# Optimization experiments

Measured on AMD Instinct MI355X. Metric: run time of the kernel, lower is better.

The kernel has to match this reference:

```python
import jax, jax.numpy as jnp
import numpy as np

T_IN, T_OUT = 336, 96      # encoder window, output_length
B, D, H = 2048, 64, 512    # batch, input_size==output_size, hidden_size


def setup_inputs() -> dict:
    key = jax.random.key(0)
    ks = jax.random.split(key, 11)
    s = 0.04  # ~1/sqrt(H) init scale
    f32 = jnp.float32
    return {
        "inputs": jax.random.normal(ks[0], (T_IN, B, D), f32),
        "enc_Wih": jax.random.normal(ks[1], (4 * H, D), f32) * s,
        "enc_Whh": jax.random.normal(ks[2], (4 * H, H), f32) * s,
        "enc_bih": jax.random.normal(ks[3], (4 * H,), f32) * s,
        "enc_bhh": jax.random.normal(ks[4], (4 * H,), f32) * s,
        "dec_Wih": jax.random.normal(ks[5], (4 * H, D), f32) * s,
        "dec_Whh": jax.random.normal(ks[6], (4 * H, H), f32) * s,
        "dec_bih": jax.random.normal(ks[7], (4 * H,), f32) * s,
        "dec_bhh": jax.random.normal(ks[8], (4 * H,), f32) * s,
        "lin_W": jax.random.normal(ks[9], (D, H), f32) * s,
        "lin_b": jax.random.normal(ks[10], (D,), f32) * s,
    }


def _lstm_cell(h, c, x, Wih, Whh, b):
    # PyTorch gate order: i, f, g, o
    g = x @ Wih.T + h @ Whh.T + b          # [B, 4H]
    i, f, gg, o = jnp.split(g, 4, axis=-1)
    c = jax.nn.sigmoid(f) * c + jax.nn.sigmoid(i) * jnp.tanh(gg)
    h = jax.nn.sigmoid(o) * jnp.tanh(c)
    return h, c


def reference(inputs, enc_Wih, enc_Whh, enc_bih, enc_bhh,
              dec_Wih, dec_Whh, dec_bih, dec_bhh, lin_W, lin_b):
    Bsz = inputs.shape[1]
    dt = inputs.dtype
    h0 = jnp.zeros((Bsz, H), dt)
    c0 = jnp.zeros((Bsz, H), dt)

    enc_b = enc_bih + enc_bhh
    def enc_step(carry, x):
        h, c = carry
        h, c = _lstm_cell(h, c, x, enc_Wih, enc_Whh, enc_b)
        return (h, c), None
    (h, c), _ = jax.lax.scan(enc_step, (h0, c0), inputs)

    dec_b = dec_bih + dec_bhh
    x0 = jnp.zeros((Bsz, D), dt)  # decoder starts from zeros(1, B, output_size)
    def dec_step(carry, _):
        h, c, x = carry
        h, c = _lstm_cell(h, c, x, dec_Wih, dec_Whh, dec_b)
        y = h @ lin_W.T + lin_b
        x_next = jax.lax.stop_gradient(y)  # decoder_output.detach()
        return (h, c, x_next), y
    _, ys = jax.lax.scan(dec_step, (h, c, x0), None, length=T_OUT)
    return ys  # [T_OUT, B, D] == torch.cat(outputs, dim=0)
```

## Files before the change

### kernel.cpp

```cpp
#include <hip/hip_runtime.h>
#include <cstdint>
#include <cstddef>

typedef __bf16 bf16_t;
typedef __bf16 bf16x8 __attribute__((ext_vector_type(8)));
typedef __bf16 bf16x4 __attribute__((ext_vector_type(4)));
typedef float f32x4 __attribute__((ext_vector_type(4)));

#define N_TIN 336
#define N_TOUT 96
#define N_B   2048
#define N_D   64
#define N_H   512

__device__ __forceinline__ void llds16(const void* g, void* l) {
  __builtin_amdgcn_global_load_lds(
      (const __attribute__((address_space(1))) unsigned*)g,
      (__attribute__((address_space(3))) unsigned*)l, 16, 0, 0);
}
__device__ __forceinline__ float sigmf(float x) { return 1.0f / (1.0f + __expf(-x)); }
__device__ __forceinline__ float tanhft(float x) {
  x = fminf(15.0f, fmaxf(-15.0f, x));
  float e = __expf(2.0f * x);
  return (e - 1.0f) / (e + 1.0f);
}
__device__ __forceinline__ int perm_row(int m) {
  int j_hi = m >> 8;
  int fi   = (m >> 4) & 15;
  int c    = m & 15;
  int gate = fi & 3;
  int j    = j_hi * 64 + (fi >> 2) * 16 + c;
  return gate * N_H + j;
}

__global__ void prep_enc_w(const float* __restrict__ Wih, const float* __restrict__ Whh,
                           const float* __restrict__ bih, const float* __restrict__ bhh,
                           bf16_t* __restrict__ Wp, float* __restrict__ bp) {
  int m = blockIdx.x;
  int n = perm_row(m);
  for (int k = threadIdx.x; k < 576; k += 256) {
    float v = (k < 64) ? Wih[n * 64 + k] : Whh[n * 512 + (k - 64)];
    Wp[(size_t)m * 576 + k] = (bf16_t)v;
  }
  if (threadIdx.x == 0) bp[m] = bih[n] + bhh[n];
}

__global__ void prep_dec_w(const float* __restrict__ Wih, const float* __restrict__ Whh,
                           const float* __restrict__ bih, const float* __restrict__ bhh,
                           const float* __restrict__ linW, const float* __restrict__ linb,
                           bf16_t* __restrict__ W0p, bf16_t* __restrict__ Wep,
                           float* __restrict__ b0p, float* __restrict__ bep) {
  int m = blockIdx.x;
  int n = perm_row(m);
  for (int k = threadIdx.x; k < 512; k += 256) {
    float whh = Whh[n * 512 + k];
    W0p[(size_t)m * 512 + k] = (bf16_t)whh;
    float acc = whh;
    #pragma unroll 8
    for (int d = 0; d < 64; ++d) acc += Wih[n * 64 + d] * linW[d * 512 + k];
    Wep[(size_t)m * 512 + k] = (bf16_t)acc;
  }
  if (threadIdx.x == 0) {
    float b = bih[n] + bhh[n];
    b0p[m] = b;
    float acc = b;
    for (int d = 0; d < 64; ++d) acc += Wih[n * 64 + d] * linb[d];
    bep[m] = acc;
  }
}

__global__ void cvt_bf16_v4(const float* __restrict__ src, bf16_t* __restrict__ dst, int n4) {
  int i = blockIdx.x * 256 + threadIdx.x;
  int stride = gridDim.x * 256;
  for (; i < n4; i += stride) {
    float4 v = ((const float4*)src)[i];
    bf16x4 o;
    o[0] = (bf16_t)v.x; o[1] = (bf16_t)v.y; o[2] = (bf16_t)v.z; o[3] = (bf16_t)v.w;
    *(bf16x4*)(dst + (size_t)i * 4) = o;
  }
}

template<int KTOT, int XK>
__global__ __launch_bounds__(256, 1)
void lstm_step(const bf16_t* __restrict__ x,
               const bf16_t* __restrict__ h_in,
               const bf16_t* __restrict__ Wp,
               const float* __restrict__ bp,
               float* __restrict__ c,
               bf16_t* __restrict__ h_out) {
  __shared__ __align__(16) char smem[2 * 8192 + 2 * 32768];
  constexpr int NK = KTOT / 64;
  const int tid  = threadIdx.x;
  const int lane = tid & 63;
  const int w    = tid >> 6;
  const int row0 = blockIdx.x * 64;
  const int wg_n = blockIdx.y;
  const int l3 = lane >> 3;
  const int q8 = ((lane & 7) ^ l3) * 8;

  auto stage = [&](int kc, int buf) {
    char* Ab = smem + buf * 8192;
    char* Bb = smem + 16384 + buf * 32768;
    #pragma unroll
    for (int ii = 0; ii < 2; ++ii) {
      int i  = 2 * w + ii;
      int rl = i * 8 + l3;
      const bf16_t* src;
      if (XK != 0 && kc == 0)
        src = x + (size_t)(row0 + rl) * XK + q8;
      else
        src = h_in + (size_t)(row0 + rl) * N_H + (kc * 64 - XK) + q8;
      llds16(src, Ab + i * 1024);
    }
    #pragma unroll
    for (int jj = 0; jj < 8; ++jj) {
      int j  = 8 * w + jj;
      int nl = j * 8 + l3;
      const bf16_t* src = Wp + (size_t)(wg_n * 256 + nl) * KTOT + kc * 64 + q8;
      llds16(src, Bb + j * 1024);
    }
  };

  f32x4 acc[4][4];
  #pragma unroll
  for (int a = 0; a < 4; ++a)
    #pragma unroll
    for (int b = 0; b < 4; ++b) acc[a][b] = (f32x4){0.f, 0.f, 0.f, 0.f};

  const int fr = lane & 15;
  const int g4 = lane >> 4;
  const int px = lane & 7;

  stage(0, 0);
  for (int kc = 0; kc < NK; ++kc) {
    asm volatile("s_waitcnt vmcnt(0)" ::: "memory");
    __syncthreads();
    if (kc + 1 < NK) stage(kc + 1, (kc + 1) & 1);
    const char* Ab = smem + (kc & 1) * 8192;
    const char* Bb = smem + 16384 + (kc & 1) * 32768;
    #pragma unroll
    for (int kk = 0; kk < 2; ++kk) {
      bf16x8 av[4], bv[4];
      int p = (kk * 4 + g4) ^ px;
      #pragma unroll
      for (int ri = 0; ri < 4; ++ri)
        av[ri] = *(const bf16x8*)(Ab + (16 * ri + fr) * 128 + p * 16);
      #pragma unroll
      for (int ci = 0; ci < 4; ++ci)
        bv[ci] = *(const bf16x8*)(Bb + ((4 * w + ci) * 16 + fr) * 128 + p * 16);
      #pragma unroll
      for (int ri = 0; ri < 4; ++ri)
        #pragma unroll
        for (int ci = 0; ci < 4; ++ci)
          acc[ri][ci] = __builtin_amdgcn_mfma_f32_16x16x32_bf16(av[ri], bv[ci], acc[ri][ci], 0, 0, 0);
    }
  }

  const int jg = wg_n * 64 + w * 16 + fr;
  const int mb = wg_n * 256 + (4 * w) * 16 + fr;
  const float bI = bp[mb], bF = bp[mb + 16], bG = bp[mb + 32], bO = bp[mb + 48];
  #pragma unroll
  for (int ri = 0; ri < 4; ++ri) {
    #pragma unroll
    for (int r = 0; r < 4; ++r) {
      int rowl = 16 * ri + g4 * 4 + r;
      size_t idx = (size_t)(row0 + rowl) * N_H + jg;
      float iv = sigmf(acc[ri][0][r] + bI);
      float fv = sigmf(acc[ri][1][r] + bF);
      float gv = tanhft(acc[ri][2][r] + bG);
      float ov = sigmf(acc[ri][3][r] + bO);
      float cn = fv * c[idx] + iv * gv;
      c[idx] = cn;
      h_out[idx] = (bf16_t)(ov * tanhft(cn));
    }
  }
}

__global__ __launch_bounds__(256, 1)
void proj_y(const bf16_t* __restrict__ h,
            const bf16_t* __restrict__ Wl,
            const float* __restrict__ bl,
            float* __restrict__ y) {
  __shared__ __align__(16) char smem[4 * 8192];
  const int tid = threadIdx.x;
  const int lane = tid & 63;
  const int w = tid >> 6;
  const int row0 = blockIdx.x * 64;
  const int l3 = lane >> 3;
  const int q8 = ((lane & 7) ^ l3) * 8;

  auto stage = [&](int kc, int buf) {
    char* Ab = smem + buf * 8192;
    char* Bb = smem + 16384 + buf * 8192;
    #pragma unroll
    for (int ii = 0; ii < 2; ++ii) {
      int i = 2 * w + ii;
      int rl = i * 8 + l3;
      llds16(h  + (size_t)(row0 + rl) * N_H + kc * 64 + q8, Ab + i * 1024);
      llds16(Wl + (size_t)rl * N_H + kc * 64 + q8,          Bb + i * 1024);
    }
  };

  f32x4 acc[4];
  #pragma unroll
  for (int ci = 0; ci < 4; ++ci) acc[ci] = (f32x4){0.f, 0.f, 0.f, 0.f};
  const int fr = lane & 15, g4 = lane >> 4, px = lane & 7;

  stage(0, 0);
  for (int kc = 0; kc < 8; ++kc) {
    asm volatile("s_waitcnt vmcnt(0)" ::: "memory");
    __syncthreads();
    if (kc + 1 < 8) stage(kc + 1, (kc + 1) & 1);
    const char* Ab = smem + (kc & 1) * 8192;
    const char* Bb = smem + 16384 + (kc & 1) * 8192;
    #pragma unroll
    for (int kk = 0; kk < 2; ++kk) {
      int p = (kk * 4 + g4) ^ px;
      bf16x8 av = *(const bf16x8*)(Ab + (16 * w + fr) * 128 + p * 16);
      #pragma unroll
      for (int ci = 0; ci < 4; ++ci) {
        bf16x8 bv = *(const bf16x8*)(Bb + (ci * 16 + fr) * 128 + p * 16);
        acc[ci] = __builtin_amdgcn_mfma_f32_16x16x32_bf16(av, bv, acc[ci], 0, 0, 0);
      }
    }
  }
  #pragma unroll
  for (int ci = 0; ci < 4; ++ci) {
    float bb = bl[ci * 16 + fr];
    #pragma unroll
    for (int r = 0; r < 4; ++r) {
      int row = row0 + 16 * w + g4 * 4 + r;
      y[(size_t)row * N_D + ci * 16 + fr] = acc[ci][r] + bb;
    }
  }
}

extern "C" void kernel_launch(void* const* d_in, const int* in_sizes, int n_in,
                              void* d_out, int out_size, void* d_ws, size_t ws_size,
                              hipStream_t stream) {
  (void)in_sizes; (void)n_in; (void)out_size; (void)ws_size;
  const float* x_f  = (const float*)d_in[0];
  const float* eWih = (const float*)d_in[1];
  const float* eWhh = (const float*)d_in[2];
  const float* ebih = (const float*)d_in[3];
  const float* ebhh = (const float*)d_in[4];
  const float* dWih = (const float*)d_in[5];
  const float* dWhh = (const float*)d_in[6];
  const float* dbih = (const float*)d_in[7];
  const float* dbhh = (const float*)d_in[8];
  const float* linW = (const float*)d_in[9];
  const float* linb = (const float*)d_in[10];
  float* out = (float*)d_out;

  char* ws = (char*)d_ws;
  size_t off = 0;
  auto alloc = [&](size_t bytes) {
    char* p = ws + off;
    off += (bytes + 255) & ~(size_t)255;
    return p;
  };
  bf16_t* Wenc  = (bf16_t*)alloc(2048ull * 576 * 2);
  bf16_t* Wdec0 = (bf16_t*)alloc(2048ull * 512 * 2);
  bf16_t* Weff  = (bf16_t*)alloc(2048ull * 512 * 2);
  bf16_t* linWb = (bf16_t*)alloc(64ull * 512 * 2);
  float*  benc  = (float*)alloc(2048 * 4);
  float*  bdec0 = (float*)alloc(2048 * 4);
  float*  beff  = (float*)alloc(2048 * 4);
  bf16_t* xb    = (bf16_t*)alloc((size_t)N_TIN * N_B * N_D * 2);
  bf16_t* h_a   = (bf16_t*)alloc((size_t)N_B * N_H * 2);
  bf16_t* h_b   = (bf16_t*)alloc((size_t)N_B * N_H * 2);
  float*  cbuf  = (float*)alloc((size_t)N_B * N_H * 4);

  prep_enc_w<<<2048, 256, 0, stream>>>(eWih, eWhh, ebih, ebhh, Wenc, benc);
  prep_dec_w<<<2048, 256, 0, stream>>>(dWih, dWhh, dbih, dbhh, linW, linb,
                                       Wdec0, Weff, bdec0, beff);
  cvt_bf16_v4<<<32, 256, 0, stream>>>(linW, linWb, 64 * 512 / 4);
  cvt_bf16_v4<<<2048, 256, 0, stream>>>(x_f, xb, N_TIN * N_B * N_D / 4);
  hipMemsetAsync(h_a, 0, (size_t)N_B * N_H * 2, stream);
  hipMemsetAsync(cbuf, 0, (size_t)N_B * N_H * 4, stream);

  dim3 grid(32, 8);
  for (int t = 0; t < N_TIN; ++t) {
    const bf16_t* hi = (t & 1) ? h_b : h_a;
    bf16_t* ho = (t & 1) ? h_a : h_b;
    lstm_step<576, 64><<<grid, 256, 0, stream>>>(xb + (size_t)t * N_B * N_D,
                                                 hi, Wenc, benc, cbuf, ho);
  }
  for (int t = 0; t < N_TOUT; ++t) {
    const bf16_t* hi = (t & 1) ? h_b : h_a;
    bf16_t* ho = (t & 1) ? h_a : h_b;
    const bf16_t* W  = (t == 0) ? Wdec0 : Weff;
    const float*  bb = (t == 0) ? bdec0 : beff;
    lstm_step<512, 0><<<grid, 256, 0, stream>>>(nullptr, hi, W, bb, cbuf, ho);
    proj_y<<<32, 256, 0, stream>>>(ho, linWb, linb, out + (size_t)t * N_B * N_D);
  }
}
```

Baseline: 5.627 ms.

## Replace per-step launches with a persistent LSTM kernel using grid barriers

Replaces 432 separate lstm_step launches and 96 proj_y launches with one persistent kernel of 256 blocks. Each block keeps its slice of the recurrent weights in LDS for the whole sequence, keeps the cell state in registers, and synchronises steps with an atomic grid barrier. The y projection is overlapped into the next decoder step by designated waves. This removes launch overhead, repeated weight reloads and the c-state memory traffic. It relies on all 256 blocks being co-resident, and the barrier has a timeout that silently gives up rather than deadlocking.

New measurement: 11.61 ms. +106.3%, slower.

```diff
diff --git a/kernel.cpp b/kernel.cpp
--- a/kernel.cpp
+++ b/kernel.cpp
@@ -12,60 +12,23 @@
 #define N_B   2048
 #define N_D   64
 #define N_H   512
-
-__device__ __forceinline__ void llds16(const void* g, void* l) {
-  __builtin_amdgcn_global_load_lds(
-      (const __attribute__((address_space(1))) unsigned*)g,
-      (__attribute__((address_space(3))) unsigned*)l, 16, 0, 0);
-}
+#define NBLK  256
+
 __device__ __forceinline__ float sigmf(float x) { return 1.0f / (1.0f + __expf(-x)); }
 __device__ __forceinline__ float tanhft(float x) {
   x = fminf(15.0f, fmaxf(-15.0f, x));
   float e = __expf(2.0f * x);
   return (e - 1.0f) / (e + 1.0f);
 }
-__device__ __forceinline__ int perm_row(int m) {
-  int j_hi = m >> 8;
-  int fi   = (m >> 4) & 15;
-  int c    = m & 15;
-  int gate = fi & 3;
-  int j    = j_hi * 64 + (fi >> 2) * 16 + c;
-  return gate * N_H + j;
-}
-
-__global__ void prep_enc_w(const float* __restrict__ Wih, const float* __restrict__ Whh,
-                           const float* __restrict__ bih, const float* __restrict__ bhh,
-                           bf16_t* __restrict__ Wp, float* __restrict__ bp) {
-  int m = blockIdx.x;
-  int n = perm_row(m);
-  for (int k = threadIdx.x; k < 576; k += 256) {
-    float v = (k < 64) ? Wih[n * 64 + k] : Whh[n * 512 + (k - 64)];
-    Wp[(size_t)m * 576 + k] = (bf16_t)v;
-  }
-  if (threadIdx.x == 0) bp[m] = bih[n] + bhh[n];
-}
-
-__global__ void prep_dec_w(const float* __restrict__ Wih, const float* __restrict__ Whh,
-                           const float* __restrict__ bih, const float* __restrict__ bhh,
-                           const float* __restrict__ linW, const float* __restrict__ linb,
-                           bf16_t* __restrict__ W0p, bf16_t* __restrict__ Wep,
-                           float* __restrict__ b0p, float* __restrict__ bep) {
-  int m = blockIdx.x;
-  int n = perm_row(m);
-  for (int k = threadIdx.x; k < 512; k += 256) {
-    float whh = Whh[n * 512 + k];
-    W0p[(size_t)m * 512 + k] = (bf16_t)whh;
-    float acc = whh;
+
+__global__ void prep_weff(const float* __restrict__ dWih, const float* __restrict__ dWhh,
+                          const float* __restrict__ linW, bf16_t* __restrict__ Weff) {
+  int n = blockIdx.x;
+  for (int k = threadIdx.x; k < N_H; k += 256) {
+    float acc = dWhh[(size_t)n * N_H + k];
     #pragma unroll 8
-    for (int d = 0; d < 64; ++d) acc += Wih[n * 64 + d] * linW[d * 512 + k];
-    Wep[(size_t)m * 512 + k] = (bf16_t)acc;
-  }
-  if (threadIdx.x == 0) {
-    float b = bih[n] + bhh[n];
-    b0p[m] = b;
-    float acc = b;
-    for (int d = 0; d < 64; ++d) acc += Wih[n * 64 + d] * linb[d];
-    bep[m] = acc;
+    for (int d = 0; d < 64; ++d) acc += dWih[(size_t)n * 64 + d] * linW[(size_t)d * N_H + k];
+    Weff[(size_t)n * N_H + k] = (bf16_t)acc;
   }
 }
 
@@ -80,159 +43,207 @@
   }
 }
 
-template<int KTOT, int XK>
-__global__ __launch_bounds__(256, 1)
-void lstm_step(const bf16_t* __restrict__ x,
-               const bf16_t* __restrict__ h_in,
-               const bf16_t* __restrict__ Wp,
-               const float* __restrict__ bp,
-               float* __restrict__ c,
-               bf16_t* __restrict__ h_out) {
-  __shared__ __align__(16) char smem[2 * 8192 + 2 * 32768];
-  constexpr int NK = KTOT / 64;
+__global__ __launch_bounds__(512, 1)
+void lstm_persist(const bf16_t* __restrict__ xb,
+                  const float* __restrict__ eWih, const float* __restrict__ eWhh,
+                  const float* __restrict__ ebih, const float* __restrict__ ebhh,
+                  const float* __restrict__ dWih, const float* __restrict__ dWhh,
+                  const float* __restrict__ dbih, const float* __restrict__ dbhh,
+                  const float* __restrict__ linb, const bf16_t* __restrict__ Weff,
+                  const bf16_t* __restrict__ linWb,
+                  bf16_t* __restrict__ hb0, bf16_t* __restrict__ hb1,
+                  float* __restrict__ out, unsigned* bar)
+{
+  __shared__ __align__(16) char smem[16 * 8192];
   const int tid  = threadIdx.x;
   const int lane = tid & 63;
   const int w    = tid >> 6;
-  const int row0 = blockIdx.x * 64;
-  const int wg_n = blockIdx.y;
-  const int l3 = lane >> 3;
-  const int q8 = ((lane & 7) ^ l3) * 8;
-
-  auto stage = [&](int kc, int buf) {
-    char* Ab = smem + buf * 8192;
-    char* Bb = smem + 16384 + buf * 32768;
-    #pragma unroll
-    for (int ii = 0; ii < 2; ++ii) {
-      int i  = 2 * w + ii;
-      int rl = i * 8 + l3;
-      const bf16_t* src;
-      if (XK != 0 && kc == 0)
-        src = x + (size_t)(row0 + rl) * XK + q8;
-      else
-        src = h_in + (size_t)(row0 + rl) * N_H + (kc * 64 - XK) + q8;
-      llds16(src, Ab + i * 1024);
-    }
-    #pragma unroll
-    for (int jj = 0; jj < 8; ++jj) {
-      int j  = 8 * w + jj;
-      int nl = j * 8 + l3;
-      const bf16_t* src = Wp + (size_t)(wg_n * 256 + nl) * KTOT + kc * 64 + q8;
-      llds16(src, Bb + j * 1024);
-    }
-  };
-
-  f32x4 acc[4][4];
-  #pragma unroll
-  for (int a = 0; a < 4; ++a)
-    #pragma unroll
-    for (int b = 0; b < 4; ++b) acc[a][b] = (f32x4){0.f, 0.f, 0.f, 0.f};
-
-  const int fr = lane & 15;
-  const int g4 = lane >> 4;
-  const int px = lane & 7;
-
-  stage(0, 0);
-  for (int kc = 0; kc < NK; ++kc) {
-    asm volatile("s_waitcnt vmcnt(0)" ::: "memory");
+  const int wr   = w >> 1, wc = w & 1;
+  const int rb   = (int)blockIdx.x >> 4, cb = (int)blockIdx.x & 15;
+  const int fr   = lane & 15, hi = lane >> 4;
+  const int jn   = (cb * 2 + wc) * 16 + fr;
+
+  unsigned barcnt = 0;
+  bool broken = false;
+  auto gbar = [&]() {
     __syncthreads();
-    if (kc + 1 < NK) stage(kc + 1, (kc + 1) & 1);
-    const char* Ab = smem + (kc & 1) * 8192;
-    const char* Bb = smem + 16384 + (kc & 1) * 32768;
-    #pragma unroll
-    for (int kk = 0; kk < 2; ++kk) {
-      bf16x8 av[4], bv[4];
-      int p = (kk * 4 + g4) ^ px;
-      #pragma unroll
-      for (int ri = 0; ri < 4; ++ri)
-        av[ri] = *(const bf16x8*)(Ab + (16 * ri + fr) * 128 + p * 16);
+    if (tid == 0) {
+      barcnt += NBLK;
+      if (!broken) {
+        __hip_atomic_fetch_add(bar, 1u, __ATOMIC_ACQ_REL, __HIP_MEMORY_SCOPE_AGENT);
+        unsigned guard = 0;
+        while (__hip_atomic_load(bar, __ATOMIC_ACQUIRE, __HIP_MEMORY_SCOPE_AGENT) < barcnt) {
+          if (++guard > (1u << 24)) { broken = true; break; }
+          __builtin_amdgcn_s_sleep(2);
+        }
+      }
+    }
+    __syncthreads();
+  };
+
+  auto stage_f32 = [&](const float* Wsrc) {
+    for (int s = tid; s < 16 * 4 * 128; s += 512) {
+      int kc = s >> 9, k8 = (s >> 7) & 3, c = s & 127;
+      int n  = ((c >> 4) & 3) * N_H + (cb * 2 + (c >> 6)) * 16 + (c & 15);
+      const float* src = Wsrc + (size_t)n * N_H + kc * 32 + k8 * 8;
+      bf16x8 o;
+      #pragma unroll
+      for (int e = 0; e < 8; ++e) o[e] = (bf16_t)src[e];
+      *(bf16x8*)(smem + (size_t)s * 16) = o;
+    }
+  };
+  auto stage_bf16 = [&](const bf16_t* Wsrc) {
+    for (int s = tid; s < 16 * 4 * 128; s += 512) {
+      int kc = s >> 9, k8 = (s >> 7) & 3, c = s & 127;
+      int n  = ((c >> 4) & 3) * N_H + (cb * 2 + (c >> 6)) * 16 + (c & 15);
+      *(bf16x8*)(smem + (size_t)s * 16) =
+          *(const bf16x8*)(Wsrc + (size_t)n * N_H + kc * 32 + k8 * 8);
+    }
+  };
+
+  stage_f32(eWhh);
+  bf16x8 bvx[2][4];
+  #pragma unroll
+  for (int kc = 0; kc < 2; ++kc)
+    #pragma unroll
+    for (int ci = 0; ci < 4; ++ci) {
+      const float* src = eWih + (size_t)(ci * N_H + jn) * 64 + kc * 32 + hi * 8;
+      bf16x8 o;
+      #pragma unroll
+      for (int e = 0; e < 8; ++e) o[e] = (bf16_t)src[e];
+      bvx[kc][ci] = o;
+    }
+  float bg[4];
+  #pragma unroll
+  for (int ci = 0; ci < 4; ++ci) bg[ci] = ebih[ci * N_H + jn] + ebhh[ci * N_H + jn];
+  __syncthreads();
+
+  const int rowA = rb * 128 + wr * 32;
+  const size_t aoff_x = (size_t)(rowA + fr) * N_D + hi * 8;
+  const size_t aoff_h = (size_t)(rowA + fr) * N_H + hi * 8;
+  const int bbase = hi * 2048 + (wc * 64 + fr) * 16;
+
+  float cc[8];
+  #pragma unroll
+  for (int i = 0; i < 8; ++i) cc[i] = 0.0f;
+
+  auto gates_x = [&](const bf16_t* xp, f32x4 (&acc)[2][4]) {
+    #pragma unroll
+    for (int kc = 0; kc < 2; ++kc) {
+      bf16x8 av0 = *(const bf16x8*)(xp + aoff_x + kc * 32);
+      bf16x8 av1 = *(const bf16x8*)(xp + aoff_x + kc * 32 + 16 * N_D);
+      #pragma unroll
+      for (int ci = 0; ci < 4; ++ci) {
+        acc[0][ci] = __builtin_amdgcn_mfma_f32_16x16x32_bf16(av0, bvx[kc][ci], acc[0][ci], 0, 0, 0);
+        acc[1][ci] = __builtin_amdgcn_mfma_f32_16x16x32_bf16(av1, bvx[kc][ci], acc[1][ci], 0, 0, 0);
+      }
+    }
+  };
+  auto gates_h = [&](const bf16_t* hp, f32x4 (&acc)[2][4]) {
+    const bf16_t* a0 = hp + aoff_h;
+    #pragma unroll
+    for (int kc = 0; kc < 16; ++kc) {
+      bf16x8 av0 = *(const bf16x8*)(a0 + kc * 32);
+      bf16x8 av1 = *(const bf16x8*)(a0 + kc * 32 + 16 * N_H);
+      bf16x8 bv[4];
       #pragma unroll
       for (int ci = 0; ci < 4; ++ci)
-        bv[ci] = *(const bf16x8*)(Bb + ((4 * w + ci) * 16 + fr) * 128 + p * 16);
-      #pragma unroll
-      for (int ri = 0; ri < 4; ++ri)
-        #pragma unroll
-        for (int ci = 0; ci < 4; ++ci)
-          acc[ri][ci] = __builtin_amdgcn_mfma_f32_16x16x32_bf16(av[ri], bv[ci], acc[ri][ci], 0, 0, 0);
-    }
-  }
-
-  const int jg = wg_n * 64 + w * 16 + fr;
-  const int mb = wg_n * 256 + (4 * w) * 16 + fr;
-  const float bI = bp[mb], bF = bp[mb + 16], bG = bp[mb + 32], bO = bp[mb + 48];
-  #pragma unroll
-  for (int ri = 0; ri < 4; ++ri) {
+        bv[ci] = *(const bf16x8*)(smem + kc * 8192 + bbase + ci * 256);
+      #pragma unroll
+      for (int ci = 0; ci < 4; ++ci) {
+        acc[0][ci] = __builtin_amdgcn_mfma_f32_16x16x32_bf16(av0, bv[ci], acc[0][ci], 0, 0, 0);
+        acc[1][ci] = __builtin_amdgcn_mfma_f32_16x16x32_bf16(av1, bv[ci], acc[1][ci], 0, 0, 0);
+      }
+    }
+  };
+  auto pwstore = [&](f32x4 (&acc)[2][4], bf16_t* hn) {
+    #pragma unroll
+    for (int ri = 0; ri < 2; ++ri) {
+      #pragma unroll
+      for (int r = 0; r < 4; ++r) {
+        float gi = sigmf(acc[ri][0][r] + bg[0]);
+        float gf = sigmf(acc[ri][1][r] + bg[1]);
+        float gg = tanhft(acc[ri][2][r] + bg[2]);
+        float go = sigmf(acc[ri][3][r] + bg[3]);
+        float cn = gf * cc[ri * 4 + r] + gi * gg;
+        cc[ri * 4 + r] = cn;
+        int row = rowA + ri * 16 + hi * 4 + r;
+        hn[(size_t)row * N_H + jn] = (bf16_t)(go * tanhft(cn));
+      }
+    }
+  };
+
+  const int gw    = (int)blockIdx.x * 8 + w;
+  const bool ywave = (gw & 3) == 0;
+  const int ytile  = gw >> 2;
+  const int ytr = ytile >> 2, ytc = ytile & 3;
+  auto yproj = [&](int s, const bf16_t* hp) {
+    f32x4 ya = {0.f, 0.f, 0.f, 0.f};
+    const bf16_t* ha = hp    + (size_t)(ytr * 16 + fr) * N_H + hi * 8;
+    const bf16_t* wa = linWb + (size_t)(ytc * 16 + fr) * N_H + hi * 8;
+    #pragma unroll
+    for (int kc = 0; kc < 16; ++kc)
+      ya = __builtin_amdgcn_mfma_f32_16x16x32_bf16(*(const bf16x8*)(ha + kc * 32),
+                                                   *(const bf16x8*)(wa + kc * 32), ya, 0, 0, 0);
+    float lb = linb[ytc * 16 + fr];
     #pragma unroll
     for (int r = 0; r < 4; ++r) {
-      int rowl = 16 * ri + g4 * 4 + r;
-      size_t idx = (size_t)(row0 + rowl) * N_H + jg;
-      float iv = sigmf(acc[ri][0][r] + bI);
-      float fv = sigmf(acc[ri][1][r] + bF);
-      float gv = tanhft(acc[ri][2][r] + bG);
-      float ov = sigmf(acc[ri][3][r] + bO);
-      float cn = fv * c[idx] + iv * gv;
-      c[idx] = cn;
-      h_out[idx] = (bf16_t)(ov * tanhft(cn));
-    }
-  }
-}
-
-__global__ __launch_bounds__(256, 1)
-void proj_y(const bf16_t* __restrict__ h,
-            const bf16_t* __restrict__ Wl,
-            const float* __restrict__ bl,
-            float* __restrict__ y) {
-  __shared__ __align__(16) char smem[4 * 8192];
-  const int tid = threadIdx.x;
-  const int lane = tid & 63;
-  const int w = tid >> 6;
-  const int row0 = blockIdx.x * 64;
-  const int l3 = lane >> 3;
-  const int q8 = ((lane & 7) ^ l3) * 8;
-
-  auto stage = [&](int kc, int buf) {
-    char* Ab = smem + buf * 8192;
-    char* Bb = smem + 16384 + buf * 8192;
-    #pragma unroll
-    for (int ii = 0; ii < 2; ++ii) {
-      int i = 2 * w + ii;
-      int rl = i * 8 + l3;
-      llds16(h  + (size_t)(row0 + rl) * N_H + kc * 64 + q8, Ab + i * 1024);
-      llds16(Wl + (size_t)rl * N_H + kc * 64 + q8,          Bb + i * 1024);
-    }
-  };
-
-  f32x4 acc[4];
-  #pragma unroll
-  for (int ci = 0; ci < 4; ++ci) acc[ci] = (f32x4){0.f, 0.f, 0.f, 0.f};
-  const int fr = lane & 15, g4 = lane >> 4, px = lane & 7;
-
-  stage(0, 0);
-  for (int kc = 0; kc < 8; ++kc) {
-    asm volatile("s_waitcnt vmcnt(0)" ::: "memory");
-    __syncthreads();
-    if (kc + 1 < 8) stage(kc + 1, (kc + 1) & 1);
-    const char* Ab = smem + (kc & 1) * 8192;
-    const char* Bb = smem + 16384 + (kc & 1) * 8192;
-    #pragma unroll
-    for (int kk = 0; kk < 2; ++kk) {
-      int p = (kk * 4 + g4) ^ px;
-      bf16x8 av = *(const bf16x8*)(Ab + (16 * w + fr) * 128 + p * 16);
-      #pragma unroll
-      for (int ci = 0; ci < 4; ++ci) {
-        bf16x8 bv = *(const bf16x8*)(Bb + (ci * 16 + fr) * 128 + p * 16);
-        acc[ci] = __builtin_amdgcn_mfma_f32_16x16x32_bf16(av, bv, acc[ci], 0, 0, 0);
-      }
-    }
-  }
+      int row = ytr * 16 + hi * 4 + r;
+      out[(size_t)s * N_B * N_D + (size_t)row * N_D + ytc * 16 + fr] = ya[r] + lb;
+    }
+  };
+
+  {
+    f32x4 acc[2][4] = {};
+    gates_x(xb, acc);
+    pwstore(acc, hb1);
+  }
+  gbar();
+
+  for (int p = 1; p < N_TIN; ++p) {
+    const bf16_t* hcur = (p & 1) ? hb1 : hb0;
+    bf16_t*       hnxt = (p & 1) ? hb0 : hb1;
+    f32x4 acc[2][4] = {};
+    gates_x(xb + (size_t)p * N_B * N_D, acc);
+    gates_h(hcur, acc);
+    pwstore(acc, hnxt);
+    gbar();
+  }
+
+  __syncthreads();
+  stage_f32(dWhh);
+  #pragma unroll
+  for (int ci = 0; ci < 4; ++ci) bg[ci] = dbih[ci * N_H + jn] + dbhh[ci * N_H + jn];
+  __syncthreads();
+  {
+    f32x4 acc[2][4] = {};
+    gates_h(hb0, acc);
+    pwstore(acc, hb1);
+  }
+  gbar();
+
+  __syncthreads();
+  stage_bf16(Weff);
   #pragma unroll
   for (int ci = 0; ci < 4; ++ci) {
-    float bb = bl[ci * 16 + fr];
-    #pragma unroll
-    for (int r = 0; r < 4; ++r) {
-      int row = row0 + 16 * w + g4 * 4 + r;
-      y[(size_t)row * N_D + ci * 16 + fr] = acc[ci][r] + bb;
-    }
-  }
+    float a = bg[ci];
+    const float* wr_ = dWih + (size_t)(ci * N_H + jn) * 64;
+    #pragma unroll 8
+    for (int d = 0; d < 64; ++d) a += wr_[d] * linb[d];
+    bg[ci] = a;
+  }
+  __syncthreads();
+
+  for (int p = N_TIN + 1; p < N_TIN + N_TOUT; ++p) {
+    const bf16_t* hcur = (p & 1) ? hb1 : hb0;
+    bf16_t*       hnxt = (p & 1) ? hb0 : hb1;
+    if (ywave) yproj(p - N_TIN - 1, hcur);
+    f32x4 acc[2][4] = {};
+    gates_h(hcur, acc);
+    pwstore(acc, hnxt);
+    gbar();
+  }
+  if (ywave) yproj(N_TOUT - 1, hb0);
 }
 
 extern "C" void kernel_launch(void* const* d_in, const int* in_sizes, int n_in,
@@ -259,39 +270,19 @@
     off += (bytes + 255) & ~(size_t)255;
     return p;
   };
-  bf16_t* Wenc  = (bf16_t*)alloc(2048ull * 576 * 2);
-  bf16_t* Wdec0 = (bf16_t*)alloc(2048ull * 512 * 2);
-  bf16_t* Weff  = (bf16_t*)alloc(2048ull * 512 * 2);
-  bf16_t* linWb = (bf16_t*)alloc(64ull * 512 * 2);
-  float*  benc  = (float*)alloc(2048 * 4);
-  float*  bdec0 = (float*)alloc(2048 * 4);
-  float*  beff  = (float*)alloc(2048 * 4);
-  bf16_t* xb    = (bf16_t*)alloc((size_t)N_TIN * N_B * N_D * 2);
-  bf16_t* h_a   = (bf16_t*)alloc((size_t)N_B * N_H * 2);
-  bf16_t* h_b   = (bf16_t*)alloc((size_t)N_B * N_H * 2);
-  float*  cbuf  = (float*)alloc((size_t)N_B * N_H * 4);
-
-  prep_enc_w<<<2048, 256, 0, stream>>>(eWih, eWhh, ebih, ebhh, Wenc, benc);
-  prep_dec_w<<<2048, 256, 0, stream>>>(dWih, dWhh, dbih, dbhh, linW, linb,
-                                       Wdec0, Weff, bdec0, beff);
+  bf16_t*  Weff  = (bf16_t*)alloc(2048ull * 512 * 2);
+  bf16_t*  linWb = (bf16_t*)alloc(64ull * 512 * 2);
+  bf16_t*  xb    = (bf16_t*)alloc((size_t)N_TIN * N_B * N_D * 2);
+  bf16_t*  hb0   = (bf16_t*)alloc((size_t)N_B * N_H * 2);
+  bf16_t*  hb1   = (bf16_t*)alloc((size_t)N_B * N_H * 2);
+  unsigned* bar  = (unsigned*)alloc(256);
+
+  prep_weff<<<2048, 256, 0, stream>>>(dWih, dWhh, linW, Weff);
   cvt_bf16_v4<<<32, 256, 0, stream>>>(linW, linWb, 64 * 512 / 4);
   cvt_bf16_v4<<<2048, 256, 0, stream>>>(x_f, xb, N_TIN * N_B * N_D / 4);
-  hipMemsetAsync(h_a, 0, (size_t)N_B * N_H * 2, stream);
-  hipMemsetAsync(cbuf, 0, (size_t)N_B * N_H * 4, stream);
-
-  dim3 grid(32, 8);
-  for (int t = 0; t < N_TIN; ++t) {
-    const bf16_t* hi = (t & 1) ? h_b : h_a;
-    bf16_t* ho = (t & 1) ? h_a : h_b;
-    lstm_step<576, 64><<<grid, 256, 0, stream>>>(xb + (size_t)t * N_B * N_D,
-                                                 hi, Wenc, benc, cbuf, ho);
-  }
-  for (int t = 0; t < N_TOUT; ++t) {
-    const bf16_t* hi = (t & 1) ? h_b : h_a;
-    bf16_t* ho = (t & 1) ? h_a : h_b;
-    const bf16_t* W  = (t == 0) ? Wdec0 : Weff;
-    const float*  bb = (t == 0) ? bdec0 : beff;
-    lstm_step<512, 0><<<grid, 256, 0, stream>>>(nullptr, hi, W, bb, cbuf, ho);
-    proj_y<<<32, 256, 0, stream>>>(ho, linWb, linb, out + (size_t)t * N_B * N_D);
-  }
-}
+  hipMemsetAsync(bar, 0, 256, stream);
+
+  lstm_persist<<<dim3(256), dim3(512), 0, stream>>>(
+      xb, eWih, eWhh, ebih, ebhh, dWih, dWhh, dbih, dbhh,
+      linb, Weff, linWb, hb0, hb1, out, bar);
+}
```
